# Kernel tuning notes

Measured on AMD Instinct MI355X. Metric: run time of the kernel, lower is better.

Reference implementation:

```python
import jax, jax.numpy as jnp
import numpy as np

B, S, H, NH = 4, 4096, 1024, 16
D = H // NH
SCALE = 1.0 / float(np.sqrt(D))


def setup_inputs() -> dict:
    key = jax.random.key(0)
    ks = jax.random.split(key, 4)
    w = 0.02
    return {
        "hidden_states": jax.random.normal(ks[0], (B, S, H), jnp.float32),
        "attention_mask": jnp.zeros((B, 1, 1, S), jnp.float32),
        "Wq": jax.random.normal(ks[1], (H, H), jnp.float32) * w,
        "bq": jnp.zeros((H,), jnp.float32),
        "Wk": jax.random.normal(ks[2], (H, H), jnp.float32) * w,
        "bk": jnp.zeros((H,), jnp.float32),
        "Wv": jax.random.normal(ks[3], (H, H), jnp.float32) * w,
        "bv": jnp.zeros((H,), jnp.float32),
    }


def reference(hidden_states, attention_mask, Wq, bq, Wk, bk, Wv, bv):
    def heads(x):  # [B,S,H] -> [B,NH,S,D]
        return x.reshape(B, S, NH, D).transpose(0, 2, 1, 3)

    q = heads(hidden_states @ Wq.T + bq)
    k = heads(hidden_states @ Wk.T + bk)
    v = heads(hidden_states @ Wv.T + bv)

    # --- global token (position 0) attends to everything ---
    gq = q[:, :, 0:1]                                   # [B,NH,1,D]
    g_scores = jnp.einsum('bhqd,bhkd->bhqk', gq, k) * SCALE + attention_mask
    g_attn = jax.nn.softmax(g_scores, axis=-1)          # [B,NH,1,S]
    g_out = jnp.einsum('bhqk,bhkd->bhqd', g_attn, v)    # [B,NH,1,D]

    # --- local tokens: 2-way attention over {own key, global key} ---
    lq = q[:, :, 1:]                                    # [B,NH,S-1,D]
    s_self = jnp.einsum('bhsd,bhsd->bhs', lq, k[:, :, 1:]) * SCALE
    s_glob = jnp.einsum('bhsd,bhd->bhs', lq, k[:, :, 0]) * SCALE
    # order matches torch cat([own, global]) along the key axis
    l_attn = jax.nn.softmax(jnp.stack([s_self, s_glob], axis=-1), axis=-1)  # [B,NH,S-1,2]
    l_out = l_attn[..., 0:1] * v[:, :, 1:] + l_attn[..., 1:2] * v[:, :, 0:1]  # [B,NH,S-1,D]

    ctx = jnp.concatenate([g_out, l_out], axis=2)       # [B,NH,S,D]
    ctx = ctx.transpose(0, 2, 1, 3).reshape(B, S, H)
    # torch returns local_attentions with shape [B,NH,S-1,1,2]
    return ctx, l_attn[:, :, :, None, :]
```

## Files before the change

kernel.cpp:

```cpp
#include <hip/hip_runtime.h>
#include <cstdint>
#include <cstddef>

#define B_   4
#define S_   4096
#define H_   1024
#define NH_  16
#define D_   64
#define M_TOT (B_ * S_)
#define K_TOT H_
#define N_TOT (3 * H_)
#define SCALE_ 0.125f
#define NCH 16
#define CH (S_ / NCH)

typedef __bf16 bf16x8 __attribute__((ext_vector_type(8)));
typedef float  f32x4  __attribute__((ext_vector_type(4)));

__device__ __forceinline__ unsigned short f2b(float x) {
    unsigned int u = __float_as_uint(x);
    u += 0x7FFFu + ((u >> 16) & 1u);
    return (unsigned short)(u >> 16);
}
__device__ __forceinline__ float b2f(unsigned int u) {
    return __uint_as_float(u << 16);
}
__device__ __forceinline__ void unp8(uint4 u, float* f) {
    f[0] = b2f(u.x & 0xffffu); f[1] = b2f(u.x >> 16);
    f[2] = b2f(u.y & 0xffffu); f[3] = b2f(u.y >> 16);
    f[4] = b2f(u.z & 0xffffu); f[5] = b2f(u.z >> 16);
    f[6] = b2f(u.w & 0xffffu); f[7] = b2f(u.w >> 16);
}

__global__ __launch_bounds__(256) void cvt_all(const float* __restrict__ hs,
                                               const float* __restrict__ wq,
                                               const float* __restrict__ wk,
                                               const float* __restrict__ wv,
                                               unsigned short* __restrict__ Xb,
                                               unsigned short* __restrict__ Wb) {
    const int i = blockIdx.x * 256 + threadIdx.x;
    const int X4 = M_TOT * K_TOT / 4;
    float4 v;
    ushort4 o;
    if (i < X4) {
        v = ((const float4*)hs)[i];
        o.x = f2b(v.x); o.y = f2b(v.y); o.z = f2b(v.z); o.w = f2b(v.w);
        ((ushort4*)Xb)[i] = o;
    } else {
        const int j = i - X4;
        const int w = j >> 18;
        const int off = j & 0x3ffff;
        const float* s = (w == 0) ? wq : (w == 1 ? wk : wv);
        v = ((const float4*)s)[off];
        o.x = f2b(v.x); o.y = f2b(v.y); o.z = f2b(v.z); o.w = f2b(v.w);
        ((ushort4*)(Wb + (size_t)w * H_ * H_))[off] = o;
    }
}

__global__ __launch_bounds__(256) void gemm_qkv(const unsigned short* __restrict__ A,
                                                const unsigned short* __restrict__ W,
                                                const float* __restrict__ bq,
                                                const float* __restrict__ bk,
                                                const float* __restrict__ bv,
                                                unsigned short* __restrict__ C) {
    __shared__ unsigned short As[128 * 32] __attribute__((aligned(16)));
    __shared__ unsigned short Bs[128 * 32] __attribute__((aligned(16)));
    const int tid  = threadIdx.x;
    const int wid  = tid >> 6;
    const int lane = tid & 63;
    const int wm = wid >> 1, wn = wid & 1;
    const int m0 = blockIdx.y * 128;
    const int n0 = blockIdx.x * 128;

    f32x4 acc[4][4];
#pragma unroll
    for (int i = 0; i < 4; i++)
#pragma unroll
        for (int j = 0; j < 4; j++) acc[i][j] = (f32x4){0.f, 0.f, 0.f, 0.f};

    const int lrow = lane >> 2;
    const int lcol = (lane & 3) * 8;

    for (int k0 = 0; k0 < K_TOT; k0 += 32) {
#pragma unroll
        for (int i = 0; i < 2; i++) {
            const int r0 = wid * 32 + i * 16;
            const unsigned short* ga = A + (size_t)(m0 + r0 + lrow) * K_TOT + k0 + lcol;
            __builtin_amdgcn_global_load_lds(
                (const __attribute__((address_space(1))) void*)ga,
                (__attribute__((address_space(3))) void*)&As[r0 * 32], 16, 0, 0);
            const unsigned short* gb = W + (size_t)(n0 + r0 + lrow) * K_TOT + k0 + lcol;
            __builtin_amdgcn_global_load_lds(
                (const __attribute__((address_space(1))) void*)gb,
                (__attribute__((address_space(3))) void*)&Bs[r0 * 32], 16, 0, 0);
        }
        __syncthreads();

        bf16x8 af[4], bfv[4];
#pragma unroll
        for (int mi = 0; mi < 4; mi++)
            af[mi] = *(const bf16x8*)&As[(wm * 64 + mi * 16 + (lane & 15)) * 32 + (lane >> 4) * 8];
#pragma unroll
        for (int ni = 0; ni < 4; ni++)
            bfv[ni] = *(const bf16x8*)&Bs[(wn * 64 + ni * 16 + (lane & 15)) * 32 + (lane >> 4) * 8];
#pragma unroll
        for (int mi = 0; mi < 4; mi++)
#pragma unroll
            for (int ni = 0; ni < 4; ni++)
                acc[mi][ni] = __builtin_amdgcn_mfma_f32_16x16x32_bf16(af[mi], bfv[ni], acc[mi][ni], 0, 0, 0);
        __syncthreads();
    }

    const int col_l = lane & 15;
    const int quad  = lane >> 4;
#pragma unroll
    for (int mi = 0; mi < 4; mi++) {
#pragma unroll
        for (int ni = 0; ni < 4; ni++) {
            const int gc = n0 + wn * 64 + ni * 16 + col_l;
            const float bias = (gc < H_) ? bq[gc] : (gc < 2 * H_ ? bk[gc - H_] : bv[gc - 2 * H_]);
#pragma unroll
            for (int i = 0; i < 4; i++) {
                const int gr = m0 + wm * 64 + mi * 16 + quad * 4 + i;
                C[(size_t)gr * N_TOT + gc] = f2b(acc[mi][ni][i] + bias);
            }
        }
    }
}

__global__ __launch_bounds__(256) void gattn_part(const unsigned short* __restrict__ QKV,
                                                  const float* __restrict__ mask,
                                                  float* __restrict__ Pm,
                                                  float* __restrict__ Pl,
                                                  float* __restrict__ Po) {
    const int bh = blockIdx.x;
    const int b = bh >> 4, h = bh & 15;
    const int chunk = blockIdx.y;
    const int tid = threadIdx.x;
    const int w = tid >> 6, lane = tid & 63;

    __shared__ float gq_sh[D_];
    __shared__ float pr[CH];
    __shared__ float red[8];
    __shared__ float osum[4][D_];

    const unsigned short* gqp = QKV + (size_t)(b * S_) * N_TOT + h * D_;
    if (tid < D_) gq_sh[tid] = b2f(gqp[tid]);
    __syncthreads();

    const int s0 = chunk * CH;
    const int s  = s0 + tid;
    const uint4* kp4 = (const uint4*)(QKV + (size_t)(b * S_ + s) * N_TOT + H_ + h * D_);
    float acc = 0.f;
#pragma unroll
    for (int c = 0; c < 8; c++) {
        uint4 r = kp4[c];
        acc += b2f(r.x & 0xffffu) * gq_sh[c * 8 + 0];
        acc += b2f(r.x >> 16)     * gq_sh[c * 8 + 1];
        acc += b2f(r.y & 0xffffu) * gq_sh[c * 8 + 2];
        acc += b2f(r.y >> 16)     * gq_sh[c * 8 + 3];
        acc += b2f(r.z & 0xffffu) * gq_sh[c * 8 + 4];
        acc += b2f(r.z >> 16)     * gq_sh[c * 8 + 5];
        acc += b2f(r.w & 0xffffu) * gq_sh[c * 8 + 6];
        acc += b2f(r.w >> 16)     * gq_sh[c * 8 + 7];
    }
    const float sv = acc * SCALE_ + mask[b * S_ + s];

    float wmax = sv;
#pragma unroll
    for (int m = 32; m >= 1; m >>= 1) wmax = fmaxf(wmax, __shfl_xor(wmax, m, 64));
    if (lane == 0) red[w] = wmax;
    __syncthreads();
    const float bmax = fmaxf(fmaxf(red[0], red[1]), fmaxf(red[2], red[3]));

    const float p = __expf(sv - bmax);
    pr[tid] = p;
    float wsum = p;
#pragma unroll
    for (int m = 32; m >= 1; m >>= 1) wsum += __shfl_xor(wsum, m, 64);
    if (lane == 0) red[4 + w] = wsum;
    __syncthreads();
    const float bsum = red[4] + red[5] + red[6] + red[7];

    float o = 0.f;
    const int sbase = s0 + w * 64;
#pragma unroll 8
    for (int i = 0; i < 64; i++) {
        const int si = sbase + i;
        const float vv = b2f((unsigned int)QKV[(size_t)(b * S_ + si) * N_TOT + 2 * H_ + h * D_ + lane]);
        o += pr[w * 64 + i] * vv;
    }
    osum[w][lane] = o;
    __syncthreads();
    if (tid < D_) {
        const float ot = osum[0][tid] + osum[1][tid] + osum[2][tid] + osum[3][tid];
        Po[(size_t)(bh * NCH + chunk) * D_ + tid] = ot;
        if (tid == 0) {
            Pm[bh * NCH + chunk] = bmax;
            Pl[bh * NCH + chunk] = bsum;
        }
    }
}

__global__ __launch_bounds__(64) void gattn_comb(const float* __restrict__ Pm,
                                                 const float* __restrict__ Pl,
                                                 const float* __restrict__ Po,
                                                 float* __restrict__ out) {
    const int bh = blockIdx.x, d = threadIdx.x;
    const int b = bh >> 4, h = bh & 15;
    float ms = -1e30f;
#pragma unroll
    for (int c = 0; c < NCH; c++) ms = fmaxf(ms, Pm[bh * NCH + c]);
    float z = 0.f, o = 0.f;
#pragma unroll
    for (int c = 0; c < NCH; c++) {
        const float e = __expf(Pm[bh * NCH + c] - ms);
        z += Pl[bh * NCH + c] * e;
        o += Po[(size_t)(bh * NCH + c) * D_ + d] * e;
    }
    out[(size_t)b * S_ * H_ + (size_t)h * D_ + d] = o / z;
}

__global__ __launch_bounds__(256) void lattn(const unsigned short* __restrict__ QKV,
                                             float* __restrict__ ctx,
                                             float* __restrict__ lat) {
    const int bh = blockIdx.x;
    const int b = bh >> 4, h = bh & 15;
    const int w = threadIdx.x >> 6, lane = threadIdx.x & 63;
    const int g = lane >> 3;
    const int l = lane & 7;
    const int s = 1 + blockIdx.y * 32 + w * 8 + g;
    if (s >= S_) return;

    const size_t rowS = (size_t)(b * S_ + s) * N_TOT + h * D_ + l * 8;
    const size_t row0 = (size_t)(b * S_) * N_TOT + h * D_ + l * 8;

    uint4 qu  = *(const uint4*)(QKV + rowS);
    uint4 ku  = *(const uint4*)(QKV + rowS + H_);
    uint4 k0u = *(const uint4*)(QKV + row0 + H_);
    float qf[8], kf[8], k0f[8];
    unp8(qu, qf); unp8(ku, kf); unp8(k0u, k0f);

    float ps = 0.f, pg = 0.f;
#pragma unroll
    for (int i = 0; i < 8; i++) { ps += qf[i] * kf[i]; pg += qf[i] * k0f[i]; }
#pragma unroll
    for (int m = 1; m < 8; m <<= 1) {
        ps += __shfl_xor(ps, m, 64);
        pg += __shfl_xor(pg, m, 64);
    }
    ps *= SCALE_; pg *= SCALE_;
    const float mx = fmaxf(ps, pg);
    const float e0 = __expf(ps - mx), e1 = __expf(pg - mx);
    const float z = e0 + e1;
    const float p0 = e0 / z, p1 = e1 / z;

    uint4 vu  = *(const uint4*)(QKV + rowS + 2 * H_);
    uint4 v0u = *(const uint4*)(QKV + row0 + 2 * H_);
    float vf[8], v0f[8];
    unp8(vu, vf); unp8(v0u, v0f);

    float* cp = ctx + (size_t)b * (S_ * H_) + (size_t)s * H_ + h * D_ + l * 8;
    float4 o0, o1;
    o0.x = p0 * vf[0] + p1 * v0f[0];
    o0.y = p0 * vf[1] + p1 * v0f[1];
    o0.z = p0 * vf[2] + p1 * v0f[2];
    o0.w = p0 * vf[3] + p1 * v0f[3];
    o1.x = p0 * vf[4] + p1 * v0f[4];
    o1.y = p0 * vf[5] + p1 * v0f[5];
    o1.z = p0 * vf[6] + p1 * v0f[6];
    o1.w = p0 * vf[7] + p1 * v0f[7];
    ((float4*)cp)[0] = o0;
    ((float4*)cp)[1] = o1;

    if (l == 0) {
        float2 lp; lp.x = p0; lp.y = p1;
        ((float2*)(lat + ((size_t)bh * (S_ - 1) + (s - 1)) * 2))[0] = lp;
    }
}

extern "C" void kernel_launch(void* const* d_in, const int* in_sizes, int n_in,
                              void* d_out, int out_size, void* d_ws, size_t ws_size,
                              hipStream_t stream) {
    const float* hs   = (const float*)d_in[0];
    const float* mask = (const float*)d_in[1];
    const float* Wq   = (const float*)d_in[2];
    const float* bq   = (const float*)d_in[3];
    const float* Wk   = (const float*)d_in[4];
    const float* bk   = (const float*)d_in[5];
    const float* Wv   = (const float*)d_in[6];
    const float* bv   = (const float*)d_in[7];

    float* out = (float*)d_out;
    float* lat = out + (size_t)B_ * S_ * H_;

    char* ws = (char*)d_ws;
    const size_t offXb  = 0;
    const size_t offWb  = offXb  + (size_t)M_TOT * K_TOT * 2;
    const size_t offQKV = offWb  + (size_t)3 * H_ * H_ * 2;
    const size_t offPm  = offQKV + (size_t)M_TOT * N_TOT * 2;
    const size_t offPl  = offPm  + (size_t)B_ * NH_ * NCH * 4;
    const size_t offPo  = offPl  + (size_t)B_ * NH_ * NCH * 4;

    unsigned short* Xb  = (unsigned short*)(ws + offXb);
    unsigned short* Wb  = (unsigned short*)(ws + offWb);
    unsigned short* QKV = (unsigned short*)(ws + offQKV);
    float* Pm = (float*)(ws + offPm);
    float* Pl = (float*)(ws + offPl);
    float* Po = (float*)(ws + offPo);

    const int total4 = M_TOT * K_TOT / 4 + 3 * H_ * H_ / 4;
    hipLaunchKernelGGL(cvt_all, dim3(total4 / 256), dim3(256), 0, stream,
                       hs, Wq, Wk, Wv, Xb, Wb);
    hipLaunchKernelGGL(gemm_qkv, dim3(N_TOT / 128, M_TOT / 128), dim3(256), 0, stream,
                       Xb, Wb, bq, bk, bv, QKV);
    hipLaunchKernelGGL(gattn_part, dim3(B_ * NH_, NCH), dim3(256), 0, stream, QKV, mask, Pm, Pl, Po);
    hipLaunchKernelGGL(gattn_comb, dim3(B_ * NH_), dim3(64), 0, stream, Pm, Pl, Po, out);
    hipLaunchKernelGGL(lattn, dim3(B_ * NH_, 128), dim3(256), 0, stream, QKV, out, lat);
}
```

Baseline: 308.8 us.

## Swizzle GEMM LDS tiles, widen conversion kernel, fold global combine into lattn

```diff
diff --git a/kernel.cpp b/kernel.cpp
--- a/kernel.cpp
+++ b/kernel.cpp
@@ -31,6 +31,9 @@
     f[4] = b2f(u.z & 0xffffu); f[5] = b2f(u.z >> 16);
     f[6] = b2f(u.w & 0xffffu); f[7] = b2f(u.w >> 16);
 }
+__device__ __forceinline__ unsigned int pack2(float lo, float hi) {
+    return (unsigned int)f2b(lo) | ((unsigned int)f2b(hi) << 16);
+}
 
 __global__ __launch_bounds__(256) void cvt_all(const float* __restrict__ hs,
                                                const float* __restrict__ wq,
@@ -39,22 +42,29 @@
                                                unsigned short* __restrict__ Xb,
                                                unsigned short* __restrict__ Wb) {
     const int i = blockIdx.x * 256 + threadIdx.x;
-    const int X4 = M_TOT * K_TOT / 4;
-    float4 v;
-    ushort4 o;
-    if (i < X4) {
-        v = ((const float4*)hs)[i];
-        o.x = f2b(v.x); o.y = f2b(v.y); o.z = f2b(v.z); o.w = f2b(v.w);
-        ((ushort4*)Xb)[i] = o;
+    const int X8 = M_TOT * K_TOT / 8;
+    const float4* sp;
+    uint4* dp;
+    int off;
+    if (i < X8) {
+        sp = (const float4*)hs;
+        dp = (uint4*)Xb;
+        off = i;
     } else {
-        const int j = i - X4;
-        const int w = j >> 18;
-        const int off = j & 0x3ffff;
-        const float* s = (w == 0) ? wq : (w == 1 ? wk : wv);
-        v = ((const float4*)s)[off];
-        o.x = f2b(v.x); o.y = f2b(v.y); o.z = f2b(v.z); o.w = f2b(v.w);
-        ((ushort4*)(Wb + (size_t)w * H_ * H_))[off] = o;
-    }
+        const int j = i - X8;
+        const int w = j >> 17;
+        off = j & 0x1ffff;
+        sp = (const float4*)((w == 0) ? wq : (w == 1 ? wk : wv));
+        dp = (uint4*)(Wb + (size_t)w * H_ * H_);
+    }
+    const float4 v0 = sp[off * 2];
+    const float4 v1 = sp[off * 2 + 1];
+    uint4 o;
+    o.x = pack2(v0.x, v0.y);
+    o.y = pack2(v0.z, v0.w);
+    o.z = pack2(v1.x, v1.y);
+    o.w = pack2(v1.z, v1.w);
+    dp[off] = o;
 }
 
 __global__ __launch_bounds__(256) void gemm_qkv(const unsigned short* __restrict__ A,
@@ -79,7 +89,10 @@
         for (int j = 0; j < 4; j++) acc[i][j] = (f32x4){0.f, 0.f, 0.f, 0.f};
 
     const int lrow = lane >> 2;
-    const int lcol = (lane & 3) * 8;
+    const int lcol = (((lane & 3) ^ ((lrow >> 1) & 3))) * 8;
+
+    const int rl    = lane & 15;
+    const int slot8 = ((lane >> 4) ^ ((rl >> 1) & 3)) * 8;
 
     for (int k0 = 0; k0 < K_TOT; k0 += 32) {
 #pragma unroll
@@ -99,10 +112,10 @@
         bf16x8 af[4], bfv[4];
 #pragma unroll
         for (int mi = 0; mi < 4; mi++)
-            af[mi] = *(const bf16x8*)&As[(wm * 64 + mi * 16 + (lane & 15)) * 32 + (lane >> 4) * 8];
+            af[mi] = *(const bf16x8*)&As[(wm * 64 + mi * 16 + rl) * 32 + slot8];
 #pragma unroll
         for (int ni = 0; ni < 4; ni++)
-            bfv[ni] = *(const bf16x8*)&Bs[(wn * 64 + ni * 16 + (lane & 15)) * 32 + (lane >> 4) * 8];
+            bfv[ni] = *(const bf16x8*)&Bs[(wn * 64 + ni * 16 + rl) * 32 + slot8];
 #pragma unroll
         for (int mi = 0; mi < 4; mi++)
 #pragma unroll
@@ -202,30 +215,33 @@
     }
 }
 
-__global__ __launch_bounds__(64) void gattn_comb(const float* __restrict__ Pm,
-                                                 const float* __restrict__ Pl,
-                                                 const float* __restrict__ Po,
-                                                 float* __restrict__ out) {
-    const int bh = blockIdx.x, d = threadIdx.x;
-    const int b = bh >> 4, h = bh & 15;
-    float ms = -1e30f;
-#pragma unroll
-    for (int c = 0; c < NCH; c++) ms = fmaxf(ms, Pm[bh * NCH + c]);
-    float z = 0.f, o = 0.f;
-#pragma unroll
-    for (int c = 0; c < NCH; c++) {
-        const float e = __expf(Pm[bh * NCH + c] - ms);
-        z += Pl[bh * NCH + c] * e;
-        o += Po[(size_t)(bh * NCH + c) * D_ + d] * e;
-    }
-    out[(size_t)b * S_ * H_ + (size_t)h * D_ + d] = o / z;
-}
-
 __global__ __launch_bounds__(256) void lattn(const unsigned short* __restrict__ QKV,
                                              float* __restrict__ ctx,
-                                             float* __restrict__ lat) {
+                                             float* __restrict__ lat,
+                                             const float* __restrict__ Pm,
+                                             const float* __restrict__ Pl,
+                                             const float* __restrict__ Po) {
     const int bh = blockIdx.x;
     const int b = bh >> 4, h = bh & 15;
+
+    if (blockIdx.y == 128) {
+        const int d = threadIdx.x;
+        if (d < D_) {
+            float ms = -1e30f;
+#pragma unroll
+            for (int c = 0; c < NCH; c++) ms = fmaxf(ms, Pm[bh * NCH + c]);
+            float z = 0.f, o = 0.f;
+#pragma unroll
+            for (int c = 0; c < NCH; c++) {
+                const float e = __expf(Pm[bh * NCH + c] - ms);
+                z += Pl[bh * NCH + c] * e;
+                o += Po[(size_t)(bh * NCH + c) * D_ + d] * e;
+            }
+            ctx[(size_t)b * S_ * H_ + (size_t)h * D_ + d] = o / z;
+        }
+        return;
+    }
+
     const int w = threadIdx.x >> 6, lane = threadIdx.x & 63;
     const int g = lane >> 3;
     const int l = lane & 7;
@@ -309,12 +325,11 @@
     float* Pl = (float*)(ws + offPl);
     float* Po = (float*)(ws + offPo);
 
-    const int total4 = M_TOT * K_TOT / 4 + 3 * H_ * H_ / 4;
-    hipLaunchKernelGGL(cvt_all, dim3(total4 / 256), dim3(256), 0, stream,
+    const int total8 = M_TOT * K_TOT / 8 + 3 * H_ * H_ / 8;
+    hipLaunchKernelGGL(cvt_all, dim3(total8 / 256), dim3(256), 0, stream,
                        hs, Wq, Wk, Wv, Xb, Wb);
     hipLaunchKernelGGL(gemm_qkv, dim3(N_TOT / 128, M_TOT / 128), dim3(256), 0, stream,
                        Xb, Wb, bq, bk, bv, QKV);
     hipLaunchKernelGGL(gattn_part, dim3(B_ * NH_, NCH), dim3(256), 0, stream, QKV, mask, Pm, Pl, Po);
-    hipLaunchKernelGGL(gattn_comb, dim3(B_ * NH_), dim3(64), 0, stream, Pm, Pl, Po, out);
-    hipLaunchKernelGGL(lattn, dim3(B_ * NH_, 128), dim3(256), 0, stream, QKV, out, lat);
-}
+    hipLaunchKernelGGL(lattn, dim3(B_ * NH_, 129), dim3(256), 0, stream, QKV, out, lat, Pm, Pl, Po);
+}
```

After: 305.9 us. Within noise of the previous version (-1.0%).
